# Performance work log

Hardware: AMD Instinct MI355X
Metric: run time of the kernel (lower is better)

## Reference

```python
import jax, jax.numpy as jnp
import numpy as np

DIM = 1024
HEADS = 16
DIM_HEAD = 64
WS = 128          # window_size
LOOK_B = 1        # look_backward
LOOK_F = 1        # look_forward (non-causal default)
SCALE = 8.0       # qk_scale (qk_rmsnorm=True)
PAD_VALUE = -1
NEG = -jnp.finfo(jnp.float32).max


def l2norm(x):
    # matches torch F.normalize(dim=-1, eps=1e-12)
    n = jnp.linalg.norm(x, axis=-1, keepdims=True)
    return x / jnp.maximum(n, 1e-12)


def rotate_half(x):
    x1, x2 = jnp.split(x, 2, axis=-1)
    return jnp.concatenate([-x2, x1], axis=-1)


def look_around(x, pad_value):
    # x: [B, w, ws, ...] -> [B, w, (LOOK_B+1+LOOK_F)*ws, ...]
    pad_width = [(0, 0)] * x.ndim
    pad_width[1] = (LOOK_B, LOOK_F)
    xp = jnp.pad(x, pad_width, constant_values=pad_value)
    w = x.shape[1]
    return jnp.concatenate([xp[:, i:i + w] for i in range(LOOK_B + LOOK_F + 1)], axis=2)


def setup_inputs() -> dict:
    key = jax.random.key(0)
    k1, k2, k3 = jax.random.split(key, 3)
    b, n = 2, 8192
    return {
        "x": jax.random.normal(k1, (b, n, DIM), dtype=jnp.float32),
        "w_qkv": jax.random.normal(k2, (DIM, 3 * HEADS * DIM_HEAD), dtype=jnp.float32) * (DIM ** -0.5),
        "w_out": jax.random.normal(k3, (HEADS * DIM_HEAD, DIM), dtype=jnp.float32) * ((HEADS * DIM_HEAD) ** -0.5),
        "q_scale": jnp.ones((DIM_HEAD,), dtype=jnp.float32),
        "k_scale": jnp.ones((DIM_HEAD,), dtype=jnp.float32),
    }


def reference(x, w_qkv, w_out, q_scale, k_scale):
    b, n, _ = x.shape
    inner = HEADS * DIM_HEAD
    qkv = x @ w_qkv                                  # [b, n, 3*inner]
    q, k, v = jnp.split(qkv, 3, axis=-1)

    def to_heads(t):
        return t.reshape(b, n, HEADS, DIM_HEAD).transpose(0, 2, 1, 3)  # [b, h, n, d]

    q, k, v = map(to_heads, (q, k, v))
    # qk rmsnorm
    q = l2norm(q) * q_scale
    k = l2norm(k) * k_scale

    # pack batch*heads; n assumed multiple of WS (autopad no-op)
    B = b * HEADS
    q, k, v = (t.reshape(B, n, DIM_HEAD) for t in (q, k, v))
    w = n // WS
    bq = q.reshape(B, w, WS, DIM_HEAD) * SCALE
    bk = look_around(k.reshape(B, w, WS, DIM_HEAD), float(PAD_VALUE))
    bv = look_around(v.reshape(B, w, WS, DIM_HEAD), float(PAD_VALUE))

    # rotary pos emb over look-around length
    seq3 = WS * (LOOK_B + 1 + LOOK_F)
    inv_freq = 1.0 / (10000.0 ** (jnp.arange(0, DIM_HEAD, 2, dtype=jnp.float32) / DIM_HEAD))
    t_pos = jnp.arange(seq3, dtype=jnp.float32)
    freqs = t_pos[:, None] * inv_freq[None, :]
    freqs = jnp.concatenate([freqs, freqs], axis=-1)   # [3ws, d]
    qf = freqs[-WS:]
    bq = bq * jnp.cos(qf) + rotate_half(bq) * jnp.sin(qf)
    bk = bk * jnp.cos(freqs) + rotate_half(bk) * jnp.sin(freqs)

    # position-based masks
    seq = jnp.arange(n, dtype=jnp.int32)
    b_t = seq.reshape(1, w, WS)
    bk_t = look_around(b_t, PAD_VALUE)                 # [1, w, 3ws]
    bq_t = b_t[..., :, None]                           # [1, w, ws, 1]
    bq_k = bk_t[..., None, :]                          # [1, w, 1, 3ws]
    pad_mask = bq_k == PAD_VALUE
    # exact_windowsize=True, non-causal
    window_mask = ((bq_k - WS * LOOK_F > bq_t)
                   | (bq_t > bq_k + WS * LOOK_B)
                   | pad_mask)

    sim = jnp.einsum('bwid,bwjd->bwij', bq, bk)        # [B, w, ws, 3ws]
    sim = jnp.where(window_mask, NEG, sim)
    attn = jax.nn.softmax(sim, axis=-1)
    out = jnp.einsum('bwij,bwjd->bwid', attn, bv)      # [B, w, ws, d]

    out = out.reshape(b, HEADS, n, DIM_HEAD).transpose(0, 2, 1, 3).reshape(b, n, inner)
    return out @ w_out
```

## Files before the change

### kernel.cpp

```cpp
#include <hip/hip_runtime.h>
#include <cstdint>
#include <cstddef>

typedef unsigned short u16;
typedef unsigned int u32;
typedef _Float16 f16;
typedef __attribute__((ext_vector_type(8))) _Float16 f16x8;
typedef __attribute__((ext_vector_type(4))) float f32x4;

#define DEV static __device__ __forceinline__

DEV u16 f2h(float f) { return __builtin_bit_cast(u16, (_Float16)f); }
DEV float h2f(u16 h) { return (float)__builtin_bit_cast(_Float16, h); }
DEV float hlo(u32 w) { return (float)__builtin_bit_cast(_Float16, (u16)(w & 0xffffu)); }
DEV float hhi(u32 w) { return (float)__builtin_bit_cast(_Float16, (u16)(w >> 16)); }
DEV u32 pk2h(float a, float b) { return (u32)f2h(a) | ((u32)f2h(b) << 16); }

#define LOG2E 1.4426950408889634f
#define NEGF (-1e30f)
#define NLOG2F (-0.41524101186092029f)

DEV float dppmax16(float x) {
    float y;
    y = __builtin_bit_cast(float, __builtin_amdgcn_mov_dpp(__builtin_bit_cast(int, x), 0xB1, 0xF, 0xF, true)); x = fmaxf(x, y);
    y = __builtin_bit_cast(float, __builtin_amdgcn_mov_dpp(__builtin_bit_cast(int, x), 0x4E, 0xF, 0xF, true)); x = fmaxf(x, y);
    y = __builtin_bit_cast(float, __builtin_amdgcn_mov_dpp(__builtin_bit_cast(int, x), 0x141, 0xF, 0xF, true)); x = fmaxf(x, y);
    y = __builtin_bit_cast(float, __builtin_amdgcn_mov_dpp(__builtin_bit_cast(int, x), 0x140, 0xF, 0xF, true)); x = fmaxf(x, y);
    return x;
}
DEV float dppsum16(float x) {
    float y;
    y = __builtin_bit_cast(float, __builtin_amdgcn_mov_dpp(__builtin_bit_cast(int, x), 0xB1, 0xF, 0xF, true)); x += y;
    y = __builtin_bit_cast(float, __builtin_amdgcn_mov_dpp(__builtin_bit_cast(int, x), 0x4E, 0xF, 0xF, true)); x += y;
    y = __builtin_bit_cast(float, __builtin_amdgcn_mov_dpp(__builtin_bit_cast(int, x), 0x141, 0xF, 0xF, true)); x += y;
    y = __builtin_bit_cast(float, __builtin_amdgcn_mov_dpp(__builtin_bit_cast(int, x), 0x140, 0xF, 0xF, true)); x += y;
    return x;
}

__global__ __launch_bounds__(256) void rope_table(float2* __restrict__ tab) {
    int idx = blockIdx.x * 256 + threadIdx.x;
    if (idx >= 384 * 32) return;
    int p = idx >> 5, d = idx & 31;
    float f = (float)p * exp2f(NLOG2F * (float)d);
    tab[idx] = make_float2(cosf(f), sinf(f));
}

__global__ __launch_bounds__(256) void cvt_f32_f16(const float* __restrict__ in,
                                                   u16* __restrict__ out, int n8) {
    int idx = blockIdx.x * 256 + threadIdx.x;
    int stride = gridDim.x * 256;
    for (int i = idx; i < n8; i += stride) {
        const float4* p = (const float4*)(in + (size_t)i * 8);
        float4 v0 = p[0], v1 = p[1];
        uint4 o;
        o.x = pk2h(v0.x, v0.y); o.y = pk2h(v0.z, v0.w);
        o.z = pk2h(v1.x, v1.y); o.w = pk2h(v1.z, v1.w);
        *(uint4*)(out + (size_t)i * 8) = o;
    }
}

__global__ __launch_bounds__(256) void transpose_cvt(const float* __restrict__ in,
                                                     u16* __restrict__ out, int R, int C) {
    __shared__ u16 t[32][33];
    int rb = blockIdx.y * 32, cb = blockIdx.x * 32;
    int x = threadIdx.x & 31, y = threadIdx.x >> 5;
#pragma unroll
    for (int yy = 0; yy < 4; ++yy) {
        int rr = y + yy * 8;
        t[x][rr] = f2h(in[(size_t)(rb + rr) * C + cb + x]);
    }
    __syncthreads();
#pragma unroll
    for (int yy = 0; yy < 4; ++yy) {
        int rr = y + yy * 8;
        out[(size_t)(cb + rr) * R + rb + x] = t[rr][x];
    }
}


DEV void gload16(const void* g, void* l) {
    __builtin_amdgcn_global_load_lds(
        (const __attribute__((address_space(1))) unsigned int*)g,
        (__attribute__((address_space(3))) unsigned int*)l, 16, 0, 0);
}

template <bool C_F32>
__global__ __launch_bounds__(256) void gemm_mfma(const u16* __restrict__ A, int lda,
                                                 const u16* __restrict__ BT, int ldb,
                                                 void* __restrict__ Cp, int ldc,
                                                 int K) {
    __shared__ __align__(16) u16 As[128 * 64];
    __shared__ __align__(16) u16 Bs[128 * 64];
    const int tid = threadIdx.x;
    const int w = tid >> 6, l = tid & 63;
    const int m0 = blockIdx.y * 128, n0 = blockIdx.x * 128;
    const int wr = (w >> 1) * 64, wc = (w & 1) * 64;
    const int r = l & 15, g = l >> 4;

    f32x4 acc[4][4] = {};

    for (int k0 = 0; k0 < K; k0 += 64) {
        __syncthreads();
#pragma unroll
        for (int i = 0; i < 4; ++i) {
            int chunk = i * 4 + w;
            int row = chunk * 8 + (l >> 3);
            int ksrc = ((l & 7) ^ (row & 7)) * 8;
            gload16(A + (size_t)(m0 + row) * lda + k0 + ksrc, &As[chunk * 512]);
            gload16(BT + (size_t)(n0 + row) * ldb + k0 + ksrc, &Bs[chunk * 512]);
        }
        __syncthreads();
#pragma unroll
        for (int kk = 0; kk < 2; ++kk) {
            f16x8 a[4], b[4];
#pragma unroll
            for (int mi = 0; mi < 4; ++mi) {
                int row = wr + mi * 16 + r;
                int byte = row * 128 + (((kk * 4 + g) ^ (row & 7)) << 4);
                a[mi] = *(const f16x8*)((const char*)As + byte);
            }
#pragma unroll
            for (int ni = 0; ni < 4; ++ni) {
                int row = wc + ni * 16 + r;
                int byte = row * 128 + (((kk * 4 + g) ^ (row & 7)) << 4);
                b[ni] = *(const f16x8*)((const char*)Bs + byte);
            }
#pragma unroll
            for (int mi = 0; mi < 4; ++mi)
#pragma unroll
                for (int ni = 0; ni < 4; ++ni)
                    acc[mi][ni] = __builtin_amdgcn_mfma_f32_16x16x32_f16(
                        a[mi], b[ni], acc[mi][ni], 0, 0, 0);
        }
    }

#pragma unroll
    for (int mi = 0; mi < 4; ++mi)
#pragma unroll
        for (int ni = 0; ni < 4; ++ni) {
            int row0 = m0 + wr + mi * 16 + g * 4;
            int col  = n0 + wc + ni * 16 + r;
#pragma unroll
            for (int rr = 0; rr < 4; ++rr) {
                size_t idx = (size_t)(row0 + rr) * ldc + col;
                if (C_F32) ((float*)Cp)[idx] = acc[mi][ni][rr];
                else       ((u16*)Cp)[idx]   = f2h(acc[mi][ni][rr]);
            }
        }
}


DEV int cmap(int c) { return c + ((c >> 5) << 2); }

__global__ __launch_bounds__(256) void gemm_nn_f32(const u16* __restrict__ A, int lda,
                                                   const float* __restrict__ B,
                                                   float* __restrict__ Cp, int ldc,
                                                   int N, int K) {
    __shared__ __align__(16) float As[16][132];
    __shared__ __align__(16) float Bs[16][140];
    const int tid = threadIdx.x;
    const int m0 = blockIdx.y * 128, n0 = blockIdx.x * 128;
    const int tx = tid & 15, ty = tid >> 4;
    const int txm = cmap(tx * 8);

    const int ar = tid >> 1, ac = (tid & 1) * 8;
    const int br = tid >> 4, bc = (tid & 15) * 8;
    const int bcm = cmap(bc);

    float acc[8][8] = {};

    for (int k0 = 0; k0 < K; k0 += 16) {
        __syncthreads();
        {
            uint4 av = *(const uint4*)(A + (size_t)(m0 + ar) * lda + k0 + ac);
            As[ac + 0][ar] = hlo(av.x); As[ac + 1][ar] = hhi(av.x);
            As[ac + 2][ar] = hlo(av.y); As[ac + 3][ar] = hhi(av.y);
            As[ac + 4][ar] = hlo(av.z); As[ac + 5][ar] = hhi(av.z);
            As[ac + 6][ar] = hlo(av.w); As[ac + 7][ar] = hhi(av.w);
        }
        {
            const float* bp = B + (size_t)(k0 + br) * N + n0 + bc;
            float4 b0 = *(const float4*)bp, b1 = *(const float4*)(bp + 4);
            *(float4*)&Bs[br][bcm]     = b0;
            *(float4*)&Bs[br][bcm + 4] = b1;
        }
        __syncthreads();
#pragma unroll
        for (int kk = 0; kk < 16; ++kk) {
            float4 a0 = *(const float4*)&As[kk][ty * 8];
            float4 a1 = *(const float4*)&As[kk][ty * 8 + 4];
            float4 b0 = *(const float4*)&Bs[kk][txm];
            float4 b1 = *(const float4*)&Bs[kk][txm + 4];
            float a[8] = {a0.x, a0.y, a0.z, a0.w, a1.x, a1.y, a1.z, a1.w};
            float b[8] = {b0.x, b0.y, b0.z, b0.w, b1.x, b1.y, b1.z, b1.w};
#pragma unroll
            for (int i = 0; i < 8; ++i)
#pragma unroll
                for (int j = 0; j < 8; ++j) acc[i][j] += a[i] * b[j];
        }
    }

#pragma unroll
    for (int i = 0; i < 8; ++i) {
        size_t row = (size_t)(m0 + ty * 8 + i);
        float* cp = Cp + row * ldc + n0 + tx * 8;
        *(float4*)cp       = make_float4(acc[i][0], acc[i][1], acc[i][2], acc[i][3]);
        *(float4*)(cp + 4) = make_float4(acc[i][4], acc[i][5], acc[i][6], acc[i][7]);
    }
}


DEV float hx(const u32* kw, int d) {
    u32 w = kw[d >> 1];
    return (d & 1) ? hhi(w) : hlo(w);
}

DEV void rope_row_h(const u16* __restrict__ src, const float2* __restrict__ r,
                    const float* __restrict__ sc, float topmul, u32* __restrict__ dst) {
    u32 kw[32];
    const uint4* p4 = (const uint4*)src;
#pragma unroll
    for (int t = 0; t < 8; ++t) {
        uint4 v = p4[t];
        kw[t*4] = v.x; kw[t*4+1] = v.y; kw[t*4+2] = v.z; kw[t*4+3] = v.w;
    }
    float ss = 0.f;
#pragma unroll
    for (int t = 0; t < 32; ++t) { float a = hlo(kw[t]), b = hhi(kw[t]); ss += a*a + b*b; }
    float inv = topmul / fmaxf(sqrtf(ss), 1e-12f);
#pragma unroll
    for (int d2 = 0; d2 < 32; d2 += 2) {
        float2 c0 = r[d2], c1 = r[d2 + 1];
        float x00 = hx(kw, d2)      * inv * sc[d2];
        float x01 = hx(kw, d2 + 32) * inv * sc[d2 + 32];
        float x10 = hx(kw, d2 + 1)  * inv * sc[d2 + 1];
        float x11 = hx(kw, d2 + 33) * inv * sc[d2 + 33];
        dst[d2 >> 1]        = pk2h(x00 * c0.x - x01 * c0.y, x10 * c1.x - x11 * c1.y);
        dst[16 + (d2 >> 1)] = pk2h(x01 * c0.x + x00 * c0.y, x11 * c1.x + x10 * c1.y);
    }
}

#define KOFF_B  18432
#define VTOFF_B 27648

__global__ __launch_bounds__(256, 2) void attn_mfma(u16* __restrict__ qkv,
                                                    const float* __restrict__ q_scale,
                                                    const float* __restrict__ k_scale,
                                                    const float2* __restrict__ rt) {
    __shared__ __align__(16) char SMB[36864];

    const int win = blockIdx.x, bh = blockIdx.y;
    const int bi = bh >> 4, h = bh & 15;
    const int tid = threadIdx.x;
    const int w = tid >> 6, l = tid & 63;
    const int r = l & 15, g = l >> 4;

    if (tid < 128) {
        const u16* src = qkv + ((size_t)(bi * 8192 + win * 128 + tid)) * 3072 + h * 64;
        rope_row_h(src, rt + (256 + tid) * 32, q_scale, 8.0f, (u32*)(SMB + tid * 144));
    }
    __syncthreads();

    f16x8 aq[2][2];
#pragma unroll
    for (int mi = 0; mi < 2; ++mi)
#pragma unroll
        for (int kk = 0; kk < 2; ++kk)
            aq[mi][kk] = *(const f16x8*)(SMB + (w * 32 + mi * 16 + r) * 144 + (kk * 4 + g) * 16);

    f32x4 acc_o[2][4] = {};
    float m[2][4], lsum[2][4];
#pragma unroll
    for (int mi = 0; mi < 2; ++mi)
#pragma unroll
        for (int rr = 0; rr < 4; ++rr) { m[mi][rr] = NEGF; lsum[mi][rr] = 0.f; }

    const int cl = (win == 0) ? 2 : 0;
    const int ch = (win == 63) ? 3 : 5;
    const int wlo = w >> 1;
    const int whi = wlo + 4;

    for (int c = cl; c <= ch; ++c) {
        __syncthreads();

        if (tid < 128) {
            int jrow = tid >> 1, hf = tid & 1;
            const u16* src = qkv + ((size_t)(bi * 8192 + (win - 1) * 128 + c * 64 + jrow)) * 3072
                             + 1024 + h * 64;
            u32 kw[32];
            const uint4* p4 = (const uint4*)src;
#pragma unroll
            for (int t = 0; t < 8; ++t) {
                uint4 v = p4[t];
                kw[t*4] = v.x; kw[t*4+1] = v.y; kw[t*4+2] = v.z; kw[t*4+3] = v.w;
            }
            float ss = 0.f;
#pragma unroll
            for (int t = 0; t < 32; ++t) { float a = hlo(kw[t]), b = hhi(kw[t]); ss += a*a + b*b; }
            float inv = 1.0f / fmaxf(sqrtf(ss), 1e-12f);
            const float2* rr_ = rt + (c * 64 + jrow) * 32;
            u32* dst = (u32*)(SMB + KOFF_B + jrow * 144 + hf * 64);
#pragma unroll
            for (int d2 = 0; d2 < 32; d2 += 2) {
                float2 c0 = rr_[d2], c1 = rr_[d2 + 1];
                float x00 = hx(kw, d2)      * inv * k_scale[d2];
                float x01 = hx(kw, d2 + 32) * inv * k_scale[d2 + 32];
                float x10 = hx(kw, d2 + 1)  * inv * k_scale[d2 + 1];
                float x11 = hx(kw, d2 + 33) * inv * k_scale[d2 + 33];
                float v0 = hf ? (x01 * c0.x + x00 * c0.y) : (x00 * c0.x - x01 * c0.y);
                float v1 = hf ? (x11 * c1.x + x10 * c1.y) : (x10 * c1.x - x11 * c1.y);
                dst[d2 >> 1] = pk2h(v0, v1);
            }
        } else {
            int tt = tid - 128;
            int jrow = tt >> 1, hf = tt & 1;
            const u16* src = qkv + ((size_t)(bi * 8192 + (win - 1) * 128 + c * 64 + jrow)) * 3072
                             + 2048 + h * 64 + hf * 32;
            u32 vw[16];
            const uint4* p4 = (const uint4*)src;
#pragma unroll
            for (int t = 0; t < 4; ++t) {
                uint4 v = p4[t];
                vw[t*4] = v.x; vw[t*4+1] = v.y; vw[t*4+2] = v.z; vw[t*4+3] = v.w;
            }
#pragma unroll
            for (int d2 = 0; d2 < 32; ++d2) {
                u16 val = (d2 & 1) ? (u16)(vw[d2 >> 1] >> 16) : (u16)(vw[d2 >> 1] & 0xffffu);
                *(u16*)(SMB + VTOFF_B + (hf * 32 + d2) * 144 + jrow * 2) = val;
            }
        }
        __syncthreads();

        if (c < wlo || c > whi) continue;

        f32x4 acc_s[2][4] = {};
#pragma unroll
        for (int kk = 0; kk < 2; ++kk) {
#pragma unroll
            for (int nj = 0; nj < 4; ++nj) {
                f16x8 bk = *(const f16x8*)(SMB + KOFF_B + (nj * 16 + r) * 144 + (kk * 4 + g) * 16);
#pragma unroll
                for (int mi = 0; mi < 2; ++mi)
                    acc_s[mi][nj] = __builtin_amdgcn_mfma_f32_16x16x32_f16(
                        aq[mi][kk], bk, acc_s[mi][nj], 0, 0, 0);
            }
        }

        float al_[2][4];
#pragma unroll
        for (int mi = 0; mi < 2; ++mi) {
#pragma unroll
            for (int rr = 0; rr < 4; ++rr) {
                const int qiw = w * 32 + mi * 16 + g * 4 + rr;
                float sv[4];
#pragma unroll
                for (int nj = 0; nj < 4; ++nj) {
                    int jp = c * 64 + nj * 16 + r;
                    bool ok = (jp >= qiw) && (jp <= qiw + 256);
                    sv[nj] = ok ? acc_s[mi][nj][rr] : NEGF;
                }
                float cm = fmaxf(fmaxf(sv[0], sv[1]), fmaxf(sv[2], sv[3]));
                cm = dppmax16(cm);
                float mn = fmaxf(m[mi][rr], cm);
                float al = exp2f((m[mi][rr] - mn) * LOG2E);
                float ps = 0.f;
#pragma unroll
                for (int nj = 0; nj < 4; ++nj) {
                    int jp = c * 64 + nj * 16 + r;
                    bool ok = (jp >= qiw) && (jp <= qiw + 256);
                    float p = ok ? exp2f((sv[nj] - mn) * LOG2E) : 0.f;
                    *(u16*)(SMB + w * 4608 + (mi * 16 + g * 4 + rr) * 144 + (nj * 16 + r) * 2) = f2h(p);
                    ps += p;
                }
                ps = dppsum16(ps);
                lsum[mi][rr] = lsum[mi][rr] * al + ps;
                m[mi][rr] = mn;
                al_[mi][rr] = al;
            }
        }
#pragma unroll
        for (int mi = 0; mi < 2; ++mi)
#pragma unroll
            for (int ni = 0; ni < 4; ++ni)
#pragma unroll
                for (int rr = 0; rr < 4; ++rr)
                    acc_o[mi][ni][rr] *= al_[mi][rr];

#pragma unroll
        for (int kkj = 0; kkj < 2; ++kkj) {
            f16x8 pa[2];
#pragma unroll
            for (int mi = 0; mi < 2; ++mi)
                pa[mi] = *(const f16x8*)(SMB + w * 4608 + (mi * 16 + r) * 144 + (kkj * 4 + g) * 16);
#pragma unroll
            for (int ni = 0; ni < 4; ++ni) {
                f16x8 bv = *(const f16x8*)(SMB + VTOFF_B + (ni * 16 + r) * 144 + (kkj * 4 + g) * 16);
#pragma unroll
                for (int mi = 0; mi < 2; ++mi)
                    acc_o[mi][ni] = __builtin_amdgcn_mfma_f32_16x16x32_f16(
                        pa[mi], bv, acc_o[mi][ni], 0, 0, 0);
            }
        }
    }

#pragma unroll
    for (int mi = 0; mi < 2; ++mi) {
        float linv[4];
#pragma unroll
        for (int rr = 0; rr < 4; ++rr) linv[rr] = 1.0f / lsum[mi][rr];
#pragma unroll
        for (int ni = 0; ni < 4; ++ni) {
#pragma unroll
            for (int rr = 0; rr < 4; ++rr) {
                int q = win * 128 + w * 32 + mi * 16 + g * 4 + rr;
                int d = ni * 16 + r;
                qkv[((size_t)(bi * 8192 + q)) * 3072 + h * 64 + d] = f2h(acc_o[mi][ni][rr] * linv[rr]);
            }
        }
    }
}


extern "C" void kernel_launch(void* const* d_in, const int* in_sizes, int n_in,
                              void* d_out, int out_size, void* d_ws, size_t ws_size,
                              hipStream_t stream) {
    const float* x       = (const float*)d_in[0];
    const float* w_qkv   = (const float*)d_in[1];
    const float* w_out   = (const float*)d_in[2];
    const float* q_scale = (const float*)d_in[3];
    const float* k_scale = (const float*)d_in[4];
    float* outp = (float*)d_out;

    u16* qkv = (u16*)d_ws;
    const size_t QKV_BYTES = 100663296;
    const size_t WOT_BYTES = 2097152;
    bool ws_has_wot = (ws_size >= QKV_BYTES + WOT_BYTES);
    u16* woT = (u16*)((char*)d_ws + QKV_BYTES);

    u16*    xh  = (u16*)d_out;
    u16*    wqT = (u16*)((char*)d_out + 33554432);
    float2* rt  = (float2*)((char*)d_out + 39845888);

    rope_table<<<dim3(48), 256, 0, stream>>>(rt);
    cvt_f32_f16<<<dim3(2048), 256, 0, stream>>>(x, xh, 2097152);
    transpose_cvt<<<dim3(96, 32), 256, 0, stream>>>(w_qkv, wqT, 1024, 3072);
    if (ws_has_wot)
        transpose_cvt<<<dim3(32, 32), 256, 0, stream>>>(w_out, woT, 1024, 1024);

    gemm_mfma<false><<<dim3(24, 128), 256, 0, stream>>>(xh, 1024, wqT, 1024, qkv, 3072, 1024);
    attn_mfma<<<dim3(64, 32), 256, 0, stream>>>(qkv, q_scale, k_scale, rt);
    if (ws_has_wot)
        gemm_mfma<true><<<dim3(8, 128), 256, 0, stream>>>(qkv, 3072, woT, 1024, outp, 1024, 1024);
    else
        gemm_nn_f32<<<dim3(8, 128), 256, 0, stream>>>(qkv, 3072, w_out, outp, 1024, 1024, 1024);
}
```

Baseline: 449.0 us.

## Fuse QK l2norm and RoPE into QKV GEMM epilogue, store V transposed

The QKV projection GEMM epilogue now applies the l2norm, scale and rotary embedding to Q and K. It writes them into a packed QK buffer and writes V transposed per head. The attention kernel then streams pre-rotated K and transposed V straight into swizzled LDS with async global-to-LDS loads, instead of redoing norm and RoPE for every window (K three times over) and transposing V through scalar LDS stores. The rope table grows to cover absolute positions and is built in double precision with fmod; occupancy hint is raised to 3 blocks. The V-transposed store in the GEMM epilogue is a strided scatter, which may cost write bandwidth.

```diff
diff --git a/kernel.cpp b/kernel.cpp
--- a/kernel.cpp
+++ b/kernel.cpp
@@ -11,14 +11,13 @@
 #define DEV static __device__ __forceinline__
 
 DEV u16 f2h(float f) { return __builtin_bit_cast(u16, (_Float16)f); }
-DEV float h2f(u16 h) { return (float)__builtin_bit_cast(_Float16, h); }
 DEV float hlo(u32 w) { return (float)__builtin_bit_cast(_Float16, (u16)(w & 0xffffu)); }
 DEV float hhi(u32 w) { return (float)__builtin_bit_cast(_Float16, (u16)(w >> 16)); }
 DEV u32 pk2h(float a, float b) { return (u32)f2h(a) | ((u32)f2h(b) << 16); }
 
 #define LOG2E 1.4426950408889634f
 #define NEGF (-1e30f)
-#define NLOG2F (-0.41524101186092029f)
+#define NLOG2F (-0.41524101186092029)
 
 DEV float dppmax16(float x) {
     float y;
@@ -37,12 +36,13 @@
     return x;
 }
 
-__global__ __launch_bounds__(256) void rope_table(float2* __restrict__ tab) {
+__global__ __launch_bounds__(256) void rope_table2(float2* __restrict__ tab) {
     int idx = blockIdx.x * 256 + threadIdx.x;
-    if (idx >= 384 * 32) return;
+    if (idx >= 8320 * 32) return;
     int p = idx >> 5, d = idx & 31;
-    float f = (float)p * exp2f(NLOG2F * (float)d);
-    tab[idx] = make_float2(cosf(f), sinf(f));
+    double th = (double)p * exp2((double)d * NLOG2F);
+    th = fmod(th, 6.283185307179586476925287);
+    tab[idx] = make_float2((float)cos(th), (float)sin(th));
 }
 
 __global__ __launch_bounds__(256) void cvt_f32_f16(const float* __restrict__ in,
@@ -82,6 +82,107 @@
     __builtin_amdgcn_global_load_lds(
         (const __attribute__((address_space(1))) unsigned int*)g,
         (__attribute__((address_space(3))) unsigned int*)l, 16, 0, 0);
+}
+
+__global__ __launch_bounds__(256) void gemm_qkv(const u16* __restrict__ A,
+                                                const u16* __restrict__ BT,
+                                                u16* __restrict__ qk,
+                                                u16* __restrict__ vt,
+                                                const float* __restrict__ q_scale,
+                                                const float* __restrict__ k_scale,
+                                                const float2* __restrict__ rt2) {
+    __shared__ __align__(16) u16 As[128 * 64];
+    __shared__ __align__(16) u16 Bs[128 * 64];
+    const int tid = threadIdx.x;
+    const int w = tid >> 6, l = tid & 63;
+    const int m0 = blockIdx.y * 128, n0 = blockIdx.x * 128;
+    const int wr = (w >> 1) * 64, wc = (w & 1) * 64;
+    const int r = l & 15, g = l >> 4;
+
+    f32x4 acc[4][4] = {};
+
+    for (int k0 = 0; k0 < 1024; k0 += 64) {
+        __syncthreads();
+#pragma unroll
+        for (int i = 0; i < 4; ++i) {
+            int chunk = i * 4 + w;
+            int row = chunk * 8 + (l >> 3);
+            int ksrc = ((l & 7) ^ (row & 7)) * 8;
+            gload16(A + (size_t)(m0 + row) * 1024 + k0 + ksrc, &As[chunk * 512]);
+            gload16(BT + (size_t)(n0 + row) * 1024 + k0 + ksrc, &Bs[chunk * 512]);
+        }
+        __syncthreads();
+#pragma unroll
+        for (int kk = 0; kk < 2; ++kk) {
+            f16x8 a[4], b[4];
+#pragma unroll
+            for (int mi = 0; mi < 4; ++mi) {
+                int row = wr + mi * 16 + r;
+                int byte = row * 128 + (((kk * 4 + g) ^ (row & 7)) << 4);
+                a[mi] = *(const f16x8*)((const char*)As + byte);
+            }
+#pragma unroll
+            for (int ni = 0; ni < 4; ++ni) {
+                int row = wc + ni * 16 + r;
+                int byte = row * 128 + (((kk * 4 + g) ^ (row & 7)) << 4);
+                b[ni] = *(const f16x8*)((const char*)Bs + byte);
+            }
+#pragma unroll
+            for (int mi = 0; mi < 4; ++mi)
+#pragma unroll
+                for (int ni = 0; ni < 4; ++ni)
+                    acc[mi][ni] = __builtin_amdgcn_mfma_f32_16x16x32_f16(
+                        a[mi], b[ni], acc[mi][ni], 0, 0, 0);
+        }
+    }
+
+    const int colbase = n0 + wc;
+    const int region = colbase >> 10;
+
+    if (region < 2) {
+        const float* sc = region ? k_scale : q_scale;
+        const float sc0 = sc[r], sc1 = sc[r + 16], sc2 = sc[r + 32], sc3 = sc[r + 48];
+        const float topmul = region ? 1.0f : 8.0f;
+        const int pshift = region ? 0 : 128;
+#pragma unroll
+        for (int mi = 0; mi < 4; ++mi) {
+#pragma unroll
+            for (int rr = 0; rr < 4; ++rr) {
+                int row = m0 + wr + mi * 16 + g * 4 + rr;
+                int nn = row & 8191;
+                float x0 = acc[mi][0][rr], x1 = acc[mi][1][rr];
+                float x2 = acc[mi][2][rr], x3 = acc[mi][3][rr];
+                float ss = x0 * x0 + x1 * x1 + x2 * x2 + x3 * x3;
+                ss = dppsum16(ss);
+                float inv = topmul / fmaxf(sqrtf(ss), 1e-12f);
+                x0 *= inv * sc0; x1 *= inv * sc1; x2 *= inv * sc2; x3 *= inv * sc3;
+                int p = nn + pshift;
+                float2 t0 = rt2[p * 32 + r];
+                float2 t1 = rt2[p * 32 + 16 + r];
+                float o0 = x0 * t0.x - x2 * t0.y, o2 = x2 * t0.x + x0 * t0.y;
+                float o1 = x1 * t1.x - x3 * t1.y, o3 = x3 * t1.x + x1 * t1.y;
+                size_t base = (size_t)row * 2048 + colbase + r;
+                qk[base]      = f2h(o0);
+                qk[base + 16] = f2h(o1);
+                qk[base + 32] = f2h(o2);
+                qk[base + 48] = f2h(o3);
+            }
+        }
+    } else {
+        const int h = (colbase & 1023) >> 6;
+#pragma unroll
+        for (int mi = 0; mi < 4; ++mi)
+#pragma unroll
+            for (int ni = 0; ni < 4; ++ni) {
+                int d = ni * 16 + r;
+#pragma unroll
+                for (int rr = 0; rr < 4; ++rr) {
+                    int row = m0 + wr + mi * 16 + g * 4 + rr;
+                    int bi = row >> 13, nn = row & 8191;
+                    vt[((size_t)((bi * 16 + h) * 64 + d)) * 8192 + nn] = f2h(acc[mi][ni][rr]);
+                }
+            }
+    }
 }
 
 template <bool C_F32>
@@ -210,44 +311,13 @@
 }
 
 
-DEV float hx(const u32* kw, int d) {
-    u32 w = kw[d >> 1];
-    return (d & 1) ? hhi(w) : hlo(w);
-}
-
-DEV void rope_row_h(const u16* __restrict__ src, const float2* __restrict__ r,
-                    const float* __restrict__ sc, float topmul, u32* __restrict__ dst) {
-    u32 kw[32];
-    const uint4* p4 = (const uint4*)src;
-#pragma unroll
-    for (int t = 0; t < 8; ++t) {
-        uint4 v = p4[t];
-        kw[t*4] = v.x; kw[t*4+1] = v.y; kw[t*4+2] = v.z; kw[t*4+3] = v.w;
-    }
-    float ss = 0.f;
-#pragma unroll
-    for (int t = 0; t < 32; ++t) { float a = hlo(kw[t]), b = hhi(kw[t]); ss += a*a + b*b; }
-    float inv = topmul / fmaxf(sqrtf(ss), 1e-12f);
-#pragma unroll
-    for (int d2 = 0; d2 < 32; d2 += 2) {
-        float2 c0 = r[d2], c1 = r[d2 + 1];
-        float x00 = hx(kw, d2)      * inv * sc[d2];
-        float x01 = hx(kw, d2 + 32) * inv * sc[d2 + 32];
-        float x10 = hx(kw, d2 + 1)  * inv * sc[d2 + 1];
-        float x11 = hx(kw, d2 + 33) * inv * sc[d2 + 33];
-        dst[d2 >> 1]        = pk2h(x00 * c0.x - x01 * c0.y, x10 * c1.x - x11 * c1.y);
-        dst[16 + (d2 >> 1)] = pk2h(x01 * c0.x + x00 * c0.y, x11 * c1.x + x10 * c1.y);
-    }
-}
-
-#define KOFF_B  18432
-#define VTOFF_B 27648
-
-__global__ __launch_bounds__(256, 2) void attn_mfma(u16* __restrict__ qkv,
-                                                    const float* __restrict__ q_scale,
-                                                    const float* __restrict__ k_scale,
-                                                    const float2* __restrict__ rt) {
-    __shared__ __align__(16) char SMB[36864];
+#define POFF  0
+#define KOFF  18432
+#define VOFF  26624
+
+__global__ __launch_bounds__(256, 3) void attn_mfma2(u16* __restrict__ qk,
+                                                     const u16* __restrict__ vt) {
+    __shared__ __align__(16) char SMB[34816];
 
     const int win = blockIdx.x, bh = blockIdx.y;
     const int bi = bh >> 4, h = bh & 15;
@@ -255,18 +325,14 @@
     const int w = tid >> 6, l = tid & 63;
     const int r = l & 15, g = l >> 4;
 
-    if (tid < 128) {
-        const u16* src = qkv + ((size_t)(bi * 8192 + win * 128 + tid)) * 3072 + h * 64;
-        rope_row_h(src, rt + (256 + tid) * 32, q_scale, 8.0f, (u32*)(SMB + tid * 144));
-    }
-    __syncthreads();
-
     f16x8 aq[2][2];
 #pragma unroll
     for (int mi = 0; mi < 2; ++mi)
 #pragma unroll
         for (int kk = 0; kk < 2; ++kk)
-            aq[mi][kk] = *(const f16x8*)(SMB + (w * 32 + mi * 16 + r) * 144 + (kk * 4 + g) * 16);
+            aq[mi][kk] = *(const f16x8*)(qk
+                + (size_t)(bi * 8192 + win * 128 + w * 32 + mi * 16 + r) * 2048
+                + h * 64 + (kk * 4 + g) * 8);
 
     f32x4 acc_o[2][4] = {};
     float m[2][4], lsum[2][4];
@@ -279,55 +345,21 @@
     const int ch = (win == 63) ? 3 : 5;
     const int wlo = w >> 1;
     const int whi = wlo + 4;
+    const size_t krow0 = (size_t)(bi * 8192 + (win - 1) * 128);
+    const size_t vrow0 = (size_t)((bi * 16 + h) * 64);
+    const int    jb0   = (win - 1) * 128;
 
     for (int c = cl; c <= ch; ++c) {
         __syncthreads();
-
-        if (tid < 128) {
-            int jrow = tid >> 1, hf = tid & 1;
-            const u16* src = qkv + ((size_t)(bi * 8192 + (win - 1) * 128 + c * 64 + jrow)) * 3072
-                             + 1024 + h * 64;
-            u32 kw[32];
-            const uint4* p4 = (const uint4*)src;
-#pragma unroll
-            for (int t = 0; t < 8; ++t) {
-                uint4 v = p4[t];
-                kw[t*4] = v.x; kw[t*4+1] = v.y; kw[t*4+2] = v.z; kw[t*4+3] = v.w;
-            }
-            float ss = 0.f;
-#pragma unroll
-            for (int t = 0; t < 32; ++t) { float a = hlo(kw[t]), b = hhi(kw[t]); ss += a*a + b*b; }
-            float inv = 1.0f / fmaxf(sqrtf(ss), 1e-12f);
-            const float2* rr_ = rt + (c * 64 + jrow) * 32;
-            u32* dst = (u32*)(SMB + KOFF_B + jrow * 144 + hf * 64);
-#pragma unroll
-            for (int d2 = 0; d2 < 32; d2 += 2) {
-                float2 c0 = rr_[d2], c1 = rr_[d2 + 1];
-                float x00 = hx(kw, d2)      * inv * k_scale[d2];
-                float x01 = hx(kw, d2 + 32) * inv * k_scale[d2 + 32];
-                float x10 = hx(kw, d2 + 1)  * inv * k_scale[d2 + 1];
-                float x11 = hx(kw, d2 + 33) * inv * k_scale[d2 + 33];
-                float v0 = hf ? (x01 * c0.x + x00 * c0.y) : (x00 * c0.x - x01 * c0.y);
-                float v1 = hf ? (x11 * c1.x + x10 * c1.y) : (x10 * c1.x - x11 * c1.y);
-                dst[d2 >> 1] = pk2h(v0, v1);
-            }
-        } else {
-            int tt = tid - 128;
-            int jrow = tt >> 1, hf = tt & 1;
-            const u16* src = qkv + ((size_t)(bi * 8192 + (win - 1) * 128 + c * 64 + jrow)) * 3072
-                             + 2048 + h * 64 + hf * 32;
-            u32 vw[16];
-            const uint4* p4 = (const uint4*)src;
-#pragma unroll
-            for (int t = 0; t < 4; ++t) {
-                uint4 v = p4[t];
-                vw[t*4] = v.x; vw[t*4+1] = v.y; vw[t*4+2] = v.z; vw[t*4+3] = v.w;
-            }
-#pragma unroll
-            for (int d2 = 0; d2 < 32; ++d2) {
-                u16 val = (d2 & 1) ? (u16)(vw[d2 >> 1] >> 16) : (u16)(vw[d2 >> 1] & 0xffffu);
-                *(u16*)(SMB + VTOFF_B + (hf * 32 + d2) * 144 + jrow * 2) = val;
-            }
+#pragma unroll
+        for (int i = 0; i < 2; ++i) {
+            int seg = w + i * 4;
+            int row = seg * 8 + (l >> 3);
+            int slot = (l & 7) ^ (row & 7);
+            gload16(qk + (krow0 + c * 64 + row) * 2048 + 1024 + h * 64 + slot * 8,
+                    SMB + KOFF + seg * 1024);
+            gload16(vt + (vrow0 + row) * 8192 + jb0 + c * 64 + slot * 8,
+                    SMB + VOFF + seg * 1024);
         }
         __syncthreads();
 
@@ -338,7 +370,9 @@
         for (int kk = 0; kk < 2; ++kk) {
 #pragma unroll
             for (int nj = 0; nj < 4; ++nj) {
-                f16x8 bk = *(const f16x8*)(SMB + KOFF_B + (nj * 16 + r) * 144 + (kk * 4 + g) * 16);
+                int row = nj * 16 + r;
+                f16x8 bk = *(const f16x8*)(SMB + KOFF + row * 128
+                                           + (((kk * 4 + g) ^ (row & 7)) << 4));
 #pragma unroll
                 for (int mi = 0; mi < 2; ++mi)
                     acc_s[mi][nj] = __builtin_amdgcn_mfma_f32_16x16x32_f16(
@@ -369,7 +403,8 @@
                     int jp = c * 64 + nj * 16 + r;
                     bool ok = (jp >= qiw) && (jp <= qiw + 256);
                     float p = ok ? exp2f((sv[nj] - mn) * LOG2E) : 0.f;
-                    *(u16*)(SMB + w * 4608 + (mi * 16 + g * 4 + rr) * 144 + (nj * 16 + r) * 2) = f2h(p);
+                    *(u16*)(SMB + POFF + w * 4608 + (mi * 16 + g * 4 + rr) * 144
+                            + (nj * 16 + r) * 2) = f2h(p);
                     ps += p;
                 }
                 ps = dppsum16(ps);
@@ -391,10 +426,13 @@
             f16x8 pa[2];
 #pragma unroll
             for (int mi = 0; mi < 2; ++mi)
-                pa[mi] = *(const f16x8*)(SMB + w * 4608 + (mi * 16 + r) * 144 + (kkj * 4 + g) * 16);
+                pa[mi] = *(const f16x8*)(SMB + POFF + w * 4608 + (mi * 16 + r) * 144
+                                         + (kkj * 4 + g) * 16);
 #pragma unroll
             for (int ni = 0; ni < 4; ++ni) {
-                f16x8 bv = *(const f16x8*)(SMB + VTOFF_B + (ni * 16 + r) * 144 + (kkj * 4 + g) * 16);
+                int row = ni * 16 + r;
+                f16x8 bv = *(const f16x8*)(SMB + VOFF + row * 128
+                                           + (((kkj * 4 + g) ^ (row & 7)) << 4));
 #pragma unroll
                 for (int mi = 0; mi < 2; ++mi)
                     acc_o[mi][ni] = __builtin_amdgcn_mfma_f32_16x16x32_f16(
@@ -409,14 +447,13 @@
 #pragma unroll
         for (int rr = 0; rr < 4; ++rr) linv[rr] = 1.0f / lsum[mi][rr];
 #pragma unroll
-        for (int ni = 0; ni < 4; ++ni) {
+        for (int ni = 0; ni < 4; ++ni)
 #pragma unroll
             for (int rr = 0; rr < 4; ++rr) {
                 int q = win * 128 + w * 32 + mi * 16 + g * 4 + rr;
-                int d = ni * 16 + r;
-                qkv[((size_t)(bi * 8192 + q)) * 3072 + h * 64 + d] = f2h(acc_o[mi][ni][rr] * linv[rr]);
-            }
-        }
+                qk[((size_t)(bi * 8192 + q)) * 2048 + h * 64 + ni * 16 + r]
+                    = f2h(acc_o[mi][ni][rr] * linv[rr]);
+            }
     }
 }
 
@@ -431,7 +468,8 @@
     const float* k_scale = (const float*)d_in[4];
     float* outp = (float*)d_out;
 
-    u16* qkv = (u16*)d_ws;
+    u16* qk = (u16*)d_ws;
+    u16* vt = (u16*)((char*)d_ws + 67108864);
     const size_t QKV_BYTES = 100663296;
     const size_t WOT_BYTES = 2097152;
     bool ws_has_wot = (ws_size >= QKV_BYTES + WOT_BYTES);
@@ -439,18 +477,18 @@
 
     u16*    xh  = (u16*)d_out;
     u16*    wqT = (u16*)((char*)d_out + 33554432);
-    float2* rt  = (float2*)((char*)d_out + 39845888);
-
-    rope_table<<<dim3(48), 256, 0, stream>>>(rt);
+    float2* rt2 = (float2*)((char*)d_out + 39845888);
+
+    rope_table2<<<dim3(1040), 256, 0, stream>>>(rt2);
     cvt_f32_f16<<<dim3(2048), 256, 0, stream>>>(x, xh, 2097152);
     transpose_cvt<<<dim3(96, 32), 256, 0, stream>>>(w_qkv, wqT, 1024, 3072);
     if (ws_has_wot)
         transpose_cvt<<<dim3(32, 32), 256, 0, stream>>>(w_out, woT, 1024, 1024);
 
-    gemm_mfma<false><<<dim3(24, 128), 256, 0, stream>>>(xh, 1024, wqT, 1024, qkv, 3072, 1024);
-    attn_mfma<<<dim3(64, 32), 256, 0, stream>>>(qkv, q_scale, k_scale, rt);
+    gemm_qkv<<<dim3(24, 128), 256, 0, stream>>>(xh, wqT, qk, vt, q_scale, k_scale, rt2);
+    attn_mfma2<<<dim3(64, 32), 256, 0, stream>>>(qk, vt);
     if (ws_has_wot)
-        gemm_mfma<true><<<dim3(8, 128), 256, 0, stream>>>(qkv, 3072, woT, 1024, outp, 1024, 1024);
+        gemm_mfma<true><<<dim3(8, 128), 256, 0, stream>>>(qk, 2048, woT, 1024, outp, 1024, 1024);
     else
-        gemm_nn_f32<<<dim3(8, 128), 256, 0, stream>>>(qkv, 3072, w_out, outp, 1024, 1024, 1024);
-}
+        gemm_nn_f32<<<dim3(8, 128), 256, 0, stream>>>(qk, 2048, w_out, outp, 1024, 1024, 1024);
+}
```

Measured after the change: 406.4 us. -9.5%, faster.
